# Kernel tuning notes

Hardware: AMD Instinct MI355X
Metric: run time of the kernel (lower is better)

The kernel has to match this reference:

```python
import jax, jax.numpy as jnp
import numpy as np

T, BS = 4, 2
C, H, W = 256, 64, 128
COUNTS = np.array([[3, 4], [2, 5], [4, 3], [3, 4]])  # [T, BS] CAVs per (timestep, sample)
N = int(COUNTS.sum())  # 28
EPS = 1e-5


def conv3x3(x, w, b):
    # x: [N,C,H,W], w: [O,I,3,3] -> SAME padding, stride 1
    y = jax.lax.conv_general_dilated(x, w, (1, 1), [(1, 1), (1, 1)],
                                     dimension_numbers=('NCHW', 'OIHW', 'NCHW'))
    return y + b[None, :, None, None]


def bn_train(x, g, b):
    # BatchNorm2d in training mode: batch statistics over (N,H,W), biased var
    m = jnp.mean(x, axis=(0, 2, 3), keepdims=True)
    v = jnp.var(x, axis=(0, 2, 3), keepdims=True)
    return (x - m) * jax.lax.rsqrt(v + EPS) * g[None, :, None, None] + b[None, :, None, None]


def setup_inputs() -> dict:
    key = jax.random.key(0)
    ks = jax.random.split(key, 6)
    seg_ids = jnp.asarray(np.repeat(np.arange(T * BS), COUNTS.reshape(-1)), dtype=jnp.int32)
    d = {
        'feature_batched': jax.random.normal(ks[0], (N, C, H, W), jnp.float32),
        # cav_fusion: Conv(256->256) + BN(256)
        'w_cav': jax.random.normal(ks[1], (C, C, 3, 3), jnp.float32) * 0.02,
        'b_cav': jnp.zeros((C,), jnp.float32), 'g_cav': jnp.ones((C,), jnp.float32), 'be_cav': jnp.zeros((C,), jnp.float32),
        # historical_fusion: Conv(256->256) + BN(256)
        'w_hist': jax.random.normal(ks[2], (C, C, 3, 3), jnp.float32) * 0.02,
        'b_hist': jnp.zeros((C,), jnp.float32), 'g_hist': jnp.ones((C,), jnp.float32), 'be_hist': jnp.zeros((C,), jnp.float32),
        # mask_model: Conv(256->64)+BN(64)+ReLU, Conv(64->1)+BN(1)+Sigmoid
        'w_m1': jax.random.normal(ks[3], (64, C, 3, 3), jnp.float32) * 0.02,
        'b_m1': jnp.zeros((64,), jnp.float32), 'g_m1': jnp.ones((64,), jnp.float32), 'be_m1': jnp.zeros((64,), jnp.float32),
        'w_m2': jax.random.normal(ks[4], (1, 64, 3, 3), jnp.float32) * 0.02,
        'b_m2': jnp.zeros((1,), jnp.float32), 'g_m2': jnp.ones((1,), jnp.float32), 'be_m2': jnp.zeros((1,), jnp.float32),
        # output_layer: Conv(256->256) + BN(256)
        'w_out': jax.random.normal(ks[5], (C, C, 3, 3), jnp.float32) * 0.02,
        'b_out': jnp.zeros((C,), jnp.float32), 'g_out': jnp.ones((C,), jnp.float32), 'be_out': jnp.zeros((C,), jnp.float32),
        'seg_ids': seg_ids,
    }
    return d


def reference(feature_batched, w_cav, b_cav, g_cav, be_cav,
              w_hist, b_hist, g_hist, be_hist,
              w_m1, b_m1, g_m1, be_m1, w_m2, b_m2, g_m2, be_m2,
              w_out, b_out, g_out, be_out, seg_ids):
    # cav_fusion over all CAV frames
    y = jax.nn.relu(bn_train(conv3x3(feature_batched, w_cav, b_cav), g_cav, be_cav))
    # ragged max-pool over variable CAV groups (timestep-major, batch-minor order)
    pooled = jax.ops.segment_max(y, seg_ids, num_segments=T * BS)
    pooled = pooled.reshape(T, BS, C, H, W)
    # cross-timestep max over historical timesteps 1..T-1
    hist = jnp.max(pooled[1:], axis=0)  # [BS,C,H,W]
    # faithful to original indexing: feature_list[bs][0] = pooled[timestep=bs, batch=0]
    base = pooled[jnp.arange(BS), 0]  # [BS,C,H,W]
    sub = jnp.min(base[None] - pooled[1:], axis=0)  # [BS,C,H,W]
    hist_out = jax.nn.relu(bn_train(conv3x3(hist, w_hist, b_hist), g_hist, be_hist))
    m = jax.nn.relu(bn_train(conv3x3(sub, w_m1, b_m1), g_m1, be_m1))
    mask = jax.nn.sigmoid(bn_train(conv3x3(m, w_m2, b_m2), g_m2, be_m2))  # [BS,1,H,W]
    fused = jax.nn.relu(bn_train(conv3x3(hist_out * mask, w_out, b_out), g_out, be_out))
    return (jnp.squeeze(mask, axis=1), fused)
```

## Files before the change

kernel.cpp:

```cpp
#include <hip/hip_runtime.h>
#include <math.h>

#define HW 8192
#define PLANE 2097152
#define EPSBN 1e-5f
#define IC28 (1.f / (28.f * 8192.f))
#define IC2  (1.f / (2.f * 8192.f))

typedef __attribute__((ext_vector_type(8))) short bh8;
typedef __attribute__((ext_vector_type(4))) float f32x4;

__device__ __constant__ int c_segOff[9] = {0, 3, 7, 9, 14, 18, 21, 24, 28};

__device__ inline ushort f2b(float f) {
    uint u = __float_as_uint(f);
    u += 0x7fff + ((u >> 16) & 1);
    return (ushort)(u >> 16);
}
__device__ inline float b2f(ushort h) { return __uint_as_float(((uint)h) << 16); }

__device__ inline void gload16(const void* g, void* l) {
    __builtin_amdgcn_global_load_lds((const __attribute__((address_space(1))) void*)g,
                                     (__attribute__((address_space(3))) void*)l, 16, 0, 0);
}

__device__ inline void bn_coef(const float* __restrict__ stats, int c, float invCnt,
                               const float* __restrict__ g, const float* __restrict__ be,
                               float& sc, float& sh)
{
    float m = stats[c] * invCnt;
    float v = stats[256 + c] * invCnt - m * m;
    sc = g[c] * rsqrtf(fmaxf(v, 0.f) + EPSBN);
    sh = be[c] - m * sc;
}

__global__ __launch_bounds__(256)
void x_transform(const float* __restrict__ x, ushort* __restrict__ xT)
{
    __shared__ float t[64 * 129];
    const int tid = threadIdx.x;
    const int c0 = blockIdx.x * 64;
    const int h = blockIdx.y;
    const int f = blockIdx.z;
    const float* src = x + (((size_t)f * 256 + c0) * 64 + h) * 128;
#pragma unroll
    for (int it = 0; it < 32; ++it) {
        int flat = it * 256 + tid;
        int ci = flat >> 7, w = flat & 127;
        t[ci * 129 + w] = src[(size_t)ci * HW + w];
    }
    __syncthreads();
    uint* dst = (uint*)(xT + ((size_t)f * HW + h * 128) * 256);
#pragma unroll
    for (int it = 0; it < 16; ++it) {
        int flat = it * 256 + tid;
        int w = flat >> 5, c2 = (flat & 31) * 2;
        uint lo = f2b(t[c2 * 129 + w]);
        uint hi = f2b(t[(c2 + 1) * 129 + w]);
        dst[w * 128 + ((c0 + c2) >> 1)] = lo | (hi << 16);
    }
}

__global__ void wgt_transform3(const float* __restrict__ w0, const float* __restrict__ w1,
                               const float* __restrict__ w2, ushort* __restrict__ wT)
{
    int z = blockIdx.y;
    const float* w = (z == 0) ? w0 : (z == 1) ? w1 : w2;
    int i = blockIdx.x * 256 + threadIdx.x;
    int co = i / 2304;
    int rem = i - co * 2304;
    int t = rem >> 8;
    int ci = rem & 255;
    wT[(size_t)z * 589824 + i] = f2b(w[((size_t)co * 256 + ci) * 9 + t]);
}

__global__ void wgt_transform(const float* __restrict__ w, ushort* __restrict__ wT,
                              int Cout, int total)
{
    int i = blockIdx.x * 256 + threadIdx.x;
    if (i >= total) return;
    int co = i / 2304;
    int rem = i - co * 2304;
    int t = rem >> 8;
    int ci = rem & 255;
    float v = (co < Cout) ? w[((size_t)co * 256 + ci) * 9 + t] : 0.f;
    wT[i] = f2b(v);
}

__global__ __launch_bounds__(256, 4)
void conv_mfma(const ushort* __restrict__ in, const ushort* __restrict__ wgtT,
               float* __restrict__ out, float* __restrict__ stats,
               const char* __restrict__ zeroPage, int Cout, int mode)
{
    __shared__ ushort As[8192];
    __shared__ ushort Bs[8192];
    const int tid = threadIdx.x;
    const int lane = tid & 63;
    const int wid = tid >> 6;
    const int wr = wid >> 1, wc = wid & 1;
    const int hRow = blockIdx.x;
    const int coBase = blockIdx.y * 128;
    const int seg = blockIdx.z;
    int f0, f1;
    if (mode) { f0 = c_segOff[seg]; f1 = c_segOff[seg + 1]; }
    else      { f0 = seg; f1 = seg + 1; }

    const int lrow = lane >> 3;
    const int lcolB = (((lane & 7) ^ lrow) << 4);

    f32x4 mx[4][4];
    float sm[4][4], sq[4][4];
#pragma unroll
    for (int m = 0; m < 4; ++m)
#pragma unroll
        for (int n = 0; n < 4; ++n) {
            mx[m][n] = (f32x4){-3.4e38f, -3.4e38f, -3.4e38f, -3.4e38f};
            sm[m][n] = 0.f; sq[m][n] = 0.f;
        }

    for (int f = f0; f < f1; ++f) {
        const ushort* inF = in + (size_t)f * HW * 256;
        f32x4 acc[4][4];
#pragma unroll
        for (int m = 0; m < 4; ++m)
#pragma unroll
            for (int n = 0; n < 4; ++n) acc[m][n] = (f32x4){0.f, 0.f, 0.f, 0.f};

        for (int t = 0; t < 9; ++t) {
            const int kh = t / 3, kw = t - kh * 3;
            const int hh = hRow + kh - 1;
            if ((unsigned)hh >= 64u) continue;
            const char* inRow = (const char*)(inF + (size_t)hh * 128 * 256);
            const char* wBase = (const char*)wgtT;
            for (int c0 = 0; c0 < 256; c0 += 64) {
                __syncthreads();
#pragma unroll
                for (int it = 0; it < 4; ++it) {
                    const int row = it * 32 + wid * 8 + lrow;
                    const char* ga = wBase +
                        (((size_t)(coBase + row) * 9 + t) * 256 + c0) * 2 + lcolB;
                    gload16(ga, (char*)As + it * 4096 + wid * 1024);
                    const int wp = row + kw - 1;
                    const char* gb = ((unsigned)wp < 128u)
                        ? inRow + ((size_t)wp * 256 + c0) * 2 + lcolB
                        : zeroPage + lcolB;
                    gload16(gb, (char*)Bs + it * 4096 + wid * 1024);
                }
                __syncthreads();
#pragma unroll
                for (int ks = 0; ks < 2; ++ks) {
                    const int koff = ks * 64 + ((lane >> 4) << 4);
                    const int sw = (lane & 7) << 4;
                    bh8 aF[4], bF[4];
#pragma unroll
                    for (int m = 0; m < 4; ++m) {
                        int r = wr * 64 + m * 16 + (lane & 15);
                        aF[m] = *(const bh8*)((const char*)As + r * 128 + (koff ^ sw));
                    }
#pragma unroll
                    for (int n = 0; n < 4; ++n) {
                        int r = wc * 64 + n * 16 + (lane & 15);
                        bF[n] = *(const bh8*)((const char*)Bs + r * 128 + (koff ^ sw));
                    }
#pragma unroll
                    for (int m = 0; m < 4; ++m)
#pragma unroll
                        for (int n = 0; n < 4; ++n)
                            acc[m][n] = __builtin_amdgcn_mfma_f32_16x16x32_bf16(
                                aF[m], bF[n], acc[m][n], 0, 0, 0);
                }
            }
        }
#pragma unroll
        for (int m = 0; m < 4; ++m)
#pragma unroll
            for (int n = 0; n < 4; ++n) {
                f32x4 a = acc[m][n];
#pragma unroll
                for (int r = 0; r < 4; ++r) {
                    sm[m][r] += a[r];
                    sq[m][r] += a[r] * a[r];
                    mx[m][n][r] = fmaxf(mx[m][n][r], a[r]);
                }
            }
    }

    const bool active = (coBase + wr * 64) < Cout;
    if (active) {
        const size_t planeBase = (size_t)seg * HW * Cout;
#pragma unroll
        for (int m = 0; m < 4; ++m) {
            int co = coBase + wr * 64 + m * 16 + ((lane >> 4) << 2);
#pragma unroll
            for (int n = 0; n < 4; ++n) {
                int px = wc * 64 + n * 16 + (lane & 15);
                float* o = out + planeBase + ((size_t)hRow * 128 + px) * Cout + co;
                *(f32x4*)o = mx[m][n];
            }
        }
#pragma unroll
        for (int m = 0; m < 4; ++m)
#pragma unroll
            for (int r = 0; r < 4; ++r) {
                float s = sm[m][r], s2 = sq[m][r];
#pragma unroll
                for (int o2 = 1; o2 < 16; o2 <<= 1) {
                    s += __shfl_xor(s, o2);
                    s2 += __shfl_xor(s2, o2);
                }
                if ((lane & 15) == 0) {
                    int co = coBase + wr * 64 + m * 16 + ((lane >> 4) << 2) + r;
                    atomicAdd(&stats[co], s);
                    atomicAdd(&stats[256 + co], s2);
                }
            }
    }
}

__global__ void pool_hist_sub(const float* __restrict__ pooled,
                              ushort* __restrict__ histB, ushort* __restrict__ subB,
                              const float* __restrict__ stats,
                              const float* __restrict__ g, const float* __restrict__ be)
{
    int i = blockIdx.x * 256 + threadIdx.x;
    int c = i & 255;
    float sc, sh;
    bn_coef(stats, c, IC28, g, be, sc, sh);
#define YP(p) fmaxf(pooled[(size_t)(p) * PLANE + i] * sc + sh, 0.f)
    float y0 = YP(0), y2 = YP(2), y3 = YP(3), y4 = YP(4), y5 = YP(5), y6 = YP(6), y7 = YP(7);
#undef YP
    float h0 = fmaxf(fmaxf(y2, y4), y6);
    float h1 = fmaxf(fmaxf(y3, y5), y7);
    histB[i] = f2b(h0);
    histB[PLANE + i] = f2b(h1);
    subB[i] = f2b(y0 - h0);
    subB[PLANE + i] = f2b(y2 - h1);
}

__global__ void bn_relu_b(const float* __restrict__ in, ushort* __restrict__ out,
                          const float* __restrict__ stats,
                          const float* __restrict__ g, const float* __restrict__ be,
                          int cMask, int total)
{
    int i = blockIdx.x * 256 + threadIdx.x;
    if (i >= total) return;
    int c = i & cMask;
    float sc, sh;
    bn_coef(stats, c, IC2, g, be, sc, sh);
    out[i] = f2b(fmaxf(in[i] * sc + sh, 0.f));
}

__global__ void mul_mask_bn(const float* __restrict__ histc, const float* __restrict__ mask,
                            ushort* __restrict__ z, const float* __restrict__ stats,
                            const float* __restrict__ g, const float* __restrict__ be)
{
    int i = blockIdx.x * 256 + threadIdx.x;
    int c = i & 255;
    int px = (i >> 8) & 8191;
    int bs = i >> 21;
    float sc, sh;
    bn_coef(stats, c, IC2, g, be, sc, sh);
    float v = fmaxf(histc[i] * sc + sh, 0.f) * mask[bs * HW + px];
    z[i] = f2b(v);
}

__global__ __launch_bounds__(256)
void conv_m2(const ushort* __restrict__ in, const float* __restrict__ w2,
             float* __restrict__ out, float* __restrict__ stats)
{
    __shared__ float wsm[576];
    int tid = threadIdx.x;
    for (int i = tid; i < 576; i += 256) wsm[i] = w2[i];
    __syncthreads();
    int idx = blockIdx.x * 256 + tid;
    int bs = idx >> 13, px = idx & 8191;
    int h = px >> 7, w = px & 127;
    const ushort* inB = in + (size_t)bs * HW * 64;
    float acc = 0.f;
#pragma unroll
    for (int kh = 0; kh < 3; ++kh) {
        int hh = h + kh - 1;
        if ((unsigned)hh >= 64u) continue;
#pragma unroll
        for (int kw = 0; kw < 3; ++kw) {
            int wp = w + kw - 1;
            if ((unsigned)wp >= 128u) continue;
            const ushort* p = inB + ((size_t)hh * 128 + wp) * 64;
            const int tbase = kh * 3 + kw;
#pragma unroll
            for (int cb = 0; cb < 64; cb += 8) {
                uint4 v = *(const uint4*)(p + cb);
                acc = fmaf(b2f((ushort)(v.x & 0xffff)), wsm[(cb + 0) * 9 + tbase], acc);
                acc = fmaf(b2f((ushort)(v.x >> 16)),    wsm[(cb + 1) * 9 + tbase], acc);
                acc = fmaf(b2f((ushort)(v.y & 0xffff)), wsm[(cb + 2) * 9 + tbase], acc);
                acc = fmaf(b2f((ushort)(v.y >> 16)),    wsm[(cb + 3) * 9 + tbase], acc);
                acc = fmaf(b2f((ushort)(v.z & 0xffff)), wsm[(cb + 4) * 9 + tbase], acc);
                acc = fmaf(b2f((ushort)(v.z >> 16)),    wsm[(cb + 5) * 9 + tbase], acc);
                acc = fmaf(b2f((ushort)(v.w & 0xffff)), wsm[(cb + 6) * 9 + tbase], acc);
                acc = fmaf(b2f((ushort)(v.w >> 16)),    wsm[(cb + 7) * 9 + tbase], acc);
            }
        }
    }
    out[idx] = acc;
    float s = acc, s2 = acc * acc;
#pragma unroll
    for (int o2 = 1; o2 < 64; o2 <<= 1) { s += __shfl_xor(s, o2); s2 += __shfl_xor(s2, o2); }
    __shared__ float red[8];
    int lane = tid & 63, wv = tid >> 6;
    if (lane == 0) { red[wv] = s; red[4 + wv] = s2; }
    __syncthreads();
    if (tid == 0) {
        atomicAdd(&stats[0], red[0] + red[1] + red[2] + red[3]);
        atomicAdd(&stats[256], red[4] + red[5] + red[6] + red[7]);
    }
}

__global__ void bn_sigmoid(const float* __restrict__ in, float* __restrict__ out,
                           const float* __restrict__ stats,
                           const float* __restrict__ g, const float* __restrict__ be)
{
    int i = blockIdx.x * 256 + threadIdx.x;
    float sc, sh;
    bn_coef(stats, 0, IC2, g, be, sc, sh);
    out[i] = 1.f / (1.f + expf(-(in[i] * sc + sh)));
}

__global__ __launch_bounds__(256)
void bn_relu_tr(const float* __restrict__ in, float* __restrict__ out,
                const float* __restrict__ stats,
                const float* __restrict__ g, const float* __restrict__ be)
{
    __shared__ float t[256 * 33];
    __shared__ float scs[256], shs[256];
    int tid = threadIdx.x;
    {
        float sc, sh;
        bn_coef(stats, tid, IC2, g, be, sc, sh);
        scs[tid] = sc; shs[tid] = sh;
    }
    __syncthreads();
    int pxBase = (blockIdx.x & 255) * 32;
    int bs = blockIdx.x >> 8;
    const float* src = in + ((size_t)bs * HW + pxBase) * 256;
#pragma unroll
    for (int it = 0; it < 32; ++it) {
        int flat = it * 256 + tid;
        int c = flat & 255, pxl = flat >> 8;
        float v = src[(size_t)pxl * 256 + c];
        t[c * 33 + pxl] = fmaxf(v * scs[c] + shs[c], 0.f);
    }
    __syncthreads();
    float* dst = out + (size_t)bs * 256 * HW + pxBase;
#pragma unroll
    for (int it = 0; it < 32; ++it) {
        int flat = it * 256 + tid;
        int pxl = flat & 31, c = flat >> 5;
        dst[(size_t)c * HW + pxl] = t[c * 33 + pxl];
    }
}

extern "C" void kernel_launch(void* const* d_in, const int* in_sizes, int n_in,
                              void* d_out, int out_size, void* d_ws, size_t ws_size,
                              hipStream_t stream)
{
    const float* x      = (const float*)d_in[0];
    const float* w_cav  = (const float*)d_in[1];
    const float* g_cav  = (const float*)d_in[3];
    const float* be_cav = (const float*)d_in[4];
    const float* w_hist = (const float*)d_in[5];
    const float* g_hist = (const float*)d_in[7];
    const float* be_hist= (const float*)d_in[8];
    const float* w_m1   = (const float*)d_in[9];
    const float* g_m1   = (const float*)d_in[11];
    const float* be_m1  = (const float*)d_in[12];
    const float* w_m2   = (const float*)d_in[13];
    const float* g_m2   = (const float*)d_in[15];
    const float* be_m2  = (const float*)d_in[16];
    const float* w_out  = (const float*)d_in[17];
    const float* g_out  = (const float*)d_in[19];
    const float* be_out = (const float*)d_in[20];

    float* ws = (float*)d_ws;
    float* outF = (float*)d_out;

    ushort* xT        = (ushort*)ws;
    ushort* wgtT_cav  = (ushort*)(ws + 29360128);
    ushort* wgtT_hist = wgtT_cav + 589824;
    ushort* wgtT_out  = wgtT_hist + 589824;
    ushort* wgtT_m1   = wgtT_out + 589824;
    float* pooled     = ws + 30392320;
    ushort* histB     = (ushort*)(ws + 47169536);
    ushort* subB      = (ushort*)(ws + 49266688);
    float* maskraw    = ws + 51363840;
    float* stats      = ws + 51380224;
    const char* zeroPage = (const char*)(stats + 2560);
    float* histc = ws;
    float* m1raw = ws + 4194304;
    ushort* mbuf = (ushort*)(ws + 5242880);
    ushort* zbuf = (ushort*)(ws + 5767168);
    float* outc  = ws + 7864320;

    hipMemsetAsync(stats, 0, 2560 * sizeof(float) + 512, stream);

    wgt_transform3<<<dim3(2304, 3), 256, 0, stream>>>(w_cav, w_hist, w_out, wgtT_cav);
    wgt_transform<<<1152, 256, 0, stream>>>(w_m1, wgtT_m1, 64, 128 * 2304);
    x_transform<<<dim3(4, 64, 28), 256, 0, stream>>>(x, xT);

    conv_mfma<<<dim3(64, 2, 8), 256, 0, stream>>>(xT, wgtT_cav, pooled,
                                                  stats + 0, zeroPage, 256, 1);
    pool_hist_sub<<<PLANE / 256, 256, 0, stream>>>(pooled, histB, subB,
                                                   stats + 0, g_cav, be_cav);

    conv_mfma<<<dim3(64, 2, 2), 256, 0, stream>>>(histB, wgtT_hist, histc,
                                                  stats + 512, zeroPage, 256, 0);

    conv_mfma<<<dim3(64, 1, 2), 256, 0, stream>>>(subB, wgtT_m1, m1raw,
                                                  stats + 1024, zeroPage, 64, 0);
    bn_relu_b<<<4096, 256, 0, stream>>>(m1raw, mbuf, stats + 1024, g_m1, be_m1,
                                        63, 2 * HW * 64);

    conv_m2<<<64, 256, 0, stream>>>(mbuf, w_m2, maskraw, stats + 1536);
    bn_sigmoid<<<64, 256, 0, stream>>>(maskraw, outF, stats + 1536, g_m2, be_m2);

    mul_mask_bn<<<16384, 256, 0, stream>>>(histc, outF, zbuf,
                                           stats + 512, g_hist, be_hist);
    conv_mfma<<<dim3(64, 2, 2), 256, 0, stream>>>(zbuf, wgtT_out, outc,
                                                  stats + 2048, zeroPage, 256, 0);
    bn_relu_tr<<<512, 256, 0, stream>>>(outc, outF + 16384,
                                        stats + 2048, g_out, be_out);
}
```

Measured before the change: 1.121 ms.

## Reuse input row tile across the three kw taps with LDS shifts

The conv kernel now loads each input row tile into LDS once per (kh, c0) step, together with weight tiles for all three kw taps. The horizontal shift is applied when fragments are read from LDS: indices are clamped and out-of-range columns are zeroed in registers, so the zero-page buffer is no longer needed. This is meant to cut global input traffic and barrier count by about three times. In exchange the weight LDS buffer triples in size and the occupancy hint drops from 4 to 2 blocks per CU.

```diff
diff --git a/kernel.cpp b/kernel.cpp
--- a/kernel.cpp
+++ b/kernel.cpp
@@ -87,12 +87,12 @@
     wT[i] = f2b(v);
 }
 
-__global__ __launch_bounds__(256, 4)
+__global__ __launch_bounds__(256, 2)
 void conv_mfma(const ushort* __restrict__ in, const ushort* __restrict__ wgtT,
                float* __restrict__ out, float* __restrict__ stats,
-               const char* __restrict__ zeroPage, int Cout, int mode)
-{
-    __shared__ ushort As[8192];
+               int Cout, int mode)
+{
+    __shared__ ushort As[3][8192];
     __shared__ ushort Bs[8192];
     const int tid = threadIdx.x;
     const int lane = tid & 63;
@@ -107,6 +107,7 @@
 
     const int lrow = lane >> 3;
     const int lcolB = (((lane & 7) ^ lrow) << 4);
+    const bh8 zero8 = {0, 0, 0, 0, 0, 0, 0, 0};
 
     f32x4 mx[4][4];
     float sm[4][4], sq[4][4];
@@ -118,6 +119,8 @@
             sm[m][n] = 0.f; sq[m][n] = 0.f;
         }
 
+    const char* wBase = (const char*)wgtT;
+
     for (int f = f0; f < f1; ++f) {
         const ushort* inF = in + (size_t)f * HW * 256;
         f32x4 acc[4][4];
@@ -126,48 +129,57 @@
 #pragma unroll
             for (int n = 0; n < 4; ++n) acc[m][n] = (f32x4){0.f, 0.f, 0.f, 0.f};
 
-        for (int t = 0; t < 9; ++t) {
-            const int kh = t / 3, kw = t - kh * 3;
+#pragma unroll
+        for (int kh = 0; kh < 3; ++kh) {
             const int hh = hRow + kh - 1;
             if ((unsigned)hh >= 64u) continue;
             const char* inRow = (const char*)(inF + (size_t)hh * 128 * 256);
-            const char* wBase = (const char*)wgtT;
             for (int c0 = 0; c0 < 256; c0 += 64) {
                 __syncthreads();
 #pragma unroll
                 for (int it = 0; it < 4; ++it) {
                     const int row = it * 32 + wid * 8 + lrow;
-                    const char* ga = wBase +
-                        (((size_t)(coBase + row) * 9 + t) * 256 + c0) * 2 + lcolB;
-                    gload16(ga, (char*)As + it * 4096 + wid * 1024);
-                    const int wp = row + kw - 1;
-                    const char* gb = ((unsigned)wp < 128u)
-                        ? inRow + ((size_t)wp * 256 + c0) * 2 + lcolB
-                        : zeroPage + lcolB;
-                    gload16(gb, (char*)Bs + it * 4096 + wid * 1024);
+                    gload16(inRow + ((size_t)row * 256 + c0) * 2 + lcolB,
+                            (char*)Bs + it * 4096 + wid * 1024);
+                }
+#pragma unroll
+                for (int kwi = 0; kwi < 3; ++kwi) {
+                    const int t = kh * 3 + kwi;
+#pragma unroll
+                    for (int it = 0; it < 4; ++it) {
+                        const int row = it * 32 + wid * 8 + lrow;
+                        gload16(wBase + (((size_t)(coBase + row) * 9 + t) * 256 + c0) * 2 + lcolB,
+                                (char*)As + kwi * 16384 + it * 4096 + wid * 1024);
+                    }
                 }
                 __syncthreads();
 #pragma unroll
-                for (int ks = 0; ks < 2; ++ks) {
-                    const int koff = ks * 64 + ((lane >> 4) << 4);
-                    const int sw = (lane & 7) << 4;
-                    bh8 aF[4], bF[4];
-#pragma unroll
-                    for (int m = 0; m < 4; ++m) {
-                        int r = wr * 64 + m * 16 + (lane & 15);
-                        aF[m] = *(const bh8*)((const char*)As + r * 128 + (koff ^ sw));
+                for (int kwi = 0; kwi < 3; ++kwi) {
+#pragma unroll
+                    for (int ks = 0; ks < 2; ++ks) {
+                        const int koff = ks * 64 + ((lane >> 4) << 4);
+                        bh8 aF[4], bF[4];
+#pragma unroll
+                        for (int m = 0; m < 4; ++m) {
+                            int r = wr * 64 + m * 16 + (lane & 15);
+                            aF[m] = *(const bh8*)((const char*)As + kwi * 16384 +
+                                                  r * 128 + (koff ^ ((lane & 7) << 4)));
+                        }
+#pragma unroll
+                        for (int n = 0; n < 4; ++n) {
+                            int rp = wc * 64 + n * 16 + (lane & 15) + kwi - 1;
+                            int rc = min(max(rp, 0), 127);
+                            bh8 v = *(const bh8*)((const char*)Bs +
+                                                  rc * 128 + (koff ^ ((rc & 7) << 4)));
+                            bF[n] = ((unsigned)rp < 128u) ? v : zero8;
+                        }
+#pragma unroll
+                        for (int m = 0; m < 4; ++m)
+#pragma unroll
+                            for (int n = 0; n < 4; ++n)
+                                acc[m][n] = __builtin_amdgcn_mfma_f32_16x16x32_bf16(
+                                    aF[m], bF[n], acc[m][n], 0, 0, 0);
                     }
-#pragma unroll
-                    for (int n = 0; n < 4; ++n) {
-                        int r = wc * 64 + n * 16 + (lane & 15);
-                        bF[n] = *(const bh8*)((const char*)Bs + r * 128 + (koff ^ sw));
-                    }
-#pragma unroll
-                    for (int m = 0; m < 4; ++m)
-#pragma unroll
-                        for (int n = 0; n < 4; ++n)
-                            acc[m][n] = __builtin_amdgcn_mfma_f32_16x16x32_bf16(
-                                aF[m], bF[n], acc[m][n], 0, 0, 0);
                 }
             }
         }
@@ -393,29 +405,28 @@
     ushort* subB      = (ushort*)(ws + 49266688);
     float* maskraw    = ws + 51363840;
     float* stats      = ws + 51380224;
-    const char* zeroPage = (const char*)(stats + 2560);
     float* histc = ws;
     float* m1raw = ws + 4194304;
     ushort* mbuf = (ushort*)(ws + 5242880);
     ushort* zbuf = (ushort*)(ws + 5767168);
     float* outc  = ws + 7864320;
 
-    hipMemsetAsync(stats, 0, 2560 * sizeof(float) + 512, stream);
+    hipMemsetAsync(stats, 0, 2560 * sizeof(float), stream);
 
     wgt_transform3<<<dim3(2304, 3), 256, 0, stream>>>(w_cav, w_hist, w_out, wgtT_cav);
     wgt_transform<<<1152, 256, 0, stream>>>(w_m1, wgtT_m1, 64, 128 * 2304);
     x_transform<<<dim3(4, 64, 28), 256, 0, stream>>>(x, xT);
 
     conv_mfma<<<dim3(64, 2, 8), 256, 0, stream>>>(xT, wgtT_cav, pooled,
-                                                  stats + 0, zeroPage, 256, 1);
+                                                  stats + 0, 256, 1);
     pool_hist_sub<<<PLANE / 256, 256, 0, stream>>>(pooled, histB, subB,
                                                    stats + 0, g_cav, be_cav);
 
     conv_mfma<<<dim3(64, 2, 2), 256, 0, stream>>>(histB, wgtT_hist, histc,
-                                                  stats + 512, zeroPage, 256, 0);
+                                                  stats + 512, 256, 0);
 
     conv_mfma<<<dim3(64, 1, 2), 256, 0, stream>>>(subB, wgtT_m1, m1raw,
-                                                  stats + 1024, zeroPage, 64, 0);
+                                                  stats + 1024, 64, 0);
     bn_relu_b<<<4096, 256, 0, stream>>>(m1raw, mbuf, stats + 1024, g_m1, be_m1,
                                         63, 2 * HW * 64);
 
@@ -425,7 +436,7 @@
     mul_mask_bn<<<16384, 256, 0, stream>>>(histc, outF, zbuf,
                                            stats + 512, g_hist, be_hist);
     conv_mfma<<<dim3(64, 2, 2), 256, 0, stream>>>(zbuf, wgtT_out, outc,
-                                                  stats + 2048, zeroPage, 256, 0);
+                                                  stats + 2048, 256, 0);
     bn_relu_tr<<<512, 256, 0, stream>>>(outc, outF + 16384,
                                         stats + 2048, g_out, be_out);
 }
```

Measured after the change: 942.0 us. -15.9%, faster.
